# Kernel tuning notes

Hardware: AMD Instinct MI355X
Metric: run time of the kernel (lower is better)

Reference implementation:

```python
import jax, jax.numpy as jnp
import numpy as np

NUM_HEADS = 8
KERNEL = 7  # odd, dilation = 1


def _neighbor_indices(n, k):
    # NATTEN semantics: window start clamped so the kxk window stays inside [0, n)
    r = k // 2
    starts = jnp.clip(jnp.arange(n) - r, 0, n - k)  # [n]
    return starts[:, None] + jnp.arange(k)[None, :]  # [n, k]


def setup_inputs() -> dict:
    key = jax.random.key(0)
    k1, k2, k3, k4 = jax.random.split(key, 4)
    B, H, W, C = 2, 56, 56, 256
    return {
        "x": jax.random.normal(k1, (B, H, W, C), dtype=jnp.float32),
        "w_qk": jax.random.normal(k2, (2 * C, C), dtype=jnp.float32) * 0.02,
        "w_v": jax.random.normal(k3, (C, C), dtype=jnp.float32) * 0.02,
        "w_proj": jax.random.normal(k4, (C, C), dtype=jnp.float32) * 0.02,
        "b_proj": jnp.zeros((C,), dtype=jnp.float32),
    }


def reference(x, w_qk, w_v, w_proj, b_proj):
    B, H, W, C = x.shape
    NH, K = NUM_HEADS, KERNEL
    HD = C // NH
    scale = HD ** -0.5

    # qk / v projections (torch Linear: y = x @ W.T)
    qk = (x @ w_qk.T).reshape(B, H, W, 2, NH, HD)
    q = jnp.moveaxis(qk[:, :, :, 0], 3, 1) * scale  # [B, NH, H, W, HD]
    k = jnp.moveaxis(qk[:, :, :, 1], 3, 1)          # [B, NH, H, W, HD]
    v = jnp.moveaxis((x @ w_v.T).reshape(B, H, W, NH, HD), 3, 1)  # [B, NH, H, W, HD]

    idx_h = _neighbor_indices(H, K)  # [H, K]
    idx_w = _neighbor_indices(W, K)  # [W, K]
    ih = idx_h[:, None, :, None]  # [H, 1, K, 1]
    iw = idx_w[None, :, None, :]  # [1, W, 1, K]

    # Gather per-pixel neighborhoods: [B, NH, H, W, K, K, HD]
    k_nb = k[:, :, ih, iw, :]
    v_nb = v[:, :, ih, iw, :]

    # windowed QK^T -> [B, NH, H, W, K*K]
    attn = jnp.einsum('bnijf,bnijpqf->bnijpq', q, k_nb).reshape(B, NH, H, W, K * K)
    attn = jax.nn.softmax(attn, axis=-1)

    # windowed AV -> [B, NH, H, W, HD]
    out = jnp.einsum('bnijk,bnijkf->bnijf', attn, v_nb.reshape(B, NH, H, W, K * K, HD))

    out = jnp.moveaxis(out, 1, 3).reshape(B, H, W, C)
    out = out @ w_proj.T + b_proj
    return out, attn
```

## Files before the change

kernel.cpp:

```cpp
#include <hip/hip_runtime.h>
#include <math.h>

#define Bb   2
#define Hh   56
#define Ww   56
#define Cc   256
#define NHh  8
#define HDd  32
#define KK   7
#define HWsz (Hh*Ww)
#define Mtot (Bb*Hh*Ww)

typedef __bf16 bf16x8 __attribute__((ext_vector_type(8)));
typedef __bf16 bf16x4 __attribute__((ext_vector_type(4)));
typedef float  f32x4  __attribute__((ext_vector_type(4)));

__global__ __launch_bounds__(256) void prep_bf16(
    const float* __restrict__ x, const float* __restrict__ wqk,
    const float* __restrict__ wv, const float* __restrict__ wp,
    __bf16* __restrict__ xb, __bf16* __restrict__ wallb, __bf16* __restrict__ wpb)
{
    const int t = blockIdx.x * 256 + threadIdx.x;
    const float* src; __bf16* dst; int off;
    if (t < 200704)      { src = x;   dst = xb;             off = t; }
    else if (t < 217088) { src = wqk; dst = wallb;          off = t - 200704; }
    else if (t < 225280) { src = wv;  dst = wallb + 131072; off = t - 217088; }
    else                 { src = wp;  dst = wpb;            off = t - 225280; }
    const int e = off * 8;
    float4 a = *(const float4*)(src + e);
    float4 b = *(const float4*)(src + e + 4);
    bf16x8 o = { (__bf16)a.x, (__bf16)a.y, (__bf16)a.z, (__bf16)a.w,
                 (__bf16)b.x, (__bf16)b.y, (__bf16)b.z, (__bf16)b.w };
    *(bf16x8*)(dst + e) = o;
}

__global__ __launch_bounds__(256) void gemm_qkv_b(
    const __bf16* __restrict__ A, const __bf16* __restrict__ Wall,
    __bf16* __restrict__ Out, float scale)
{
    __shared__ __bf16 As[4096];
    __shared__ __bf16 Bs[4096];

    const int Kdim = 256;
    const int tid = threadIdx.x;
    const int bid = blockIdx.x;
    const int swz = (bid & 7) * 147 + (bid >> 3);
    const int m0  = (swz / 12) * 64;
    const int n0  = (swz % 12) * 64;

    const int mm = tid >> 2;
    const int q  = tid & 3;
    const __bf16* arow = A    + (size_t)(m0 + mm) * Kdim + q * 16;
    const __bf16* brow = Wall + (size_t)(n0 + mm) * Kdim + q * 16;

    const int ks_st  = q >> 1;
    const int sub_st = mm >> 4;
    const int row_st = mm & 15;
    const int c0_st  = (q & 1) * 2;
    const int blk_st = ks_st * 4 + sub_st;
    const int off0 = blk_st * 512 + row_st * 32 + ((c0_st ^ (row_st & 3)) * 8);
    const int off1 = blk_st * 512 + row_st * 32 + (((c0_st + 1) ^ (row_st & 3)) * 8);

    const int w    = tid >> 6;
    const int lane = tid & 63;
    const int fr_row = lane & 15;
    const int fr_c   = lane >> 4;
    const int fr_off = fr_row * 32 + ((fr_c ^ (fr_row & 3)) * 8);

    f32x4 acc[4] = {};

    for (int k0 = 0; k0 < Kdim; k0 += 64) {
        bf16x8 av0 = *(const bf16x8*)(arow + k0);
        bf16x8 av1 = *(const bf16x8*)(arow + k0 + 8);
        bf16x8 bv0 = *(const bf16x8*)(brow + k0);
        bf16x8 bv1 = *(const bf16x8*)(brow + k0 + 8);
        __syncthreads();
        *(bf16x8*)&As[off0] = av0;
        *(bf16x8*)&As[off1] = av1;
        *(bf16x8*)&Bs[off0] = bv0;
        *(bf16x8*)&Bs[off1] = bv1;
        __syncthreads();
        #pragma unroll
        for (int ks = 0; ks < 2; ++ks) {
            bf16x8 af = *(const bf16x8*)&As[(ks * 4 + w) * 512 + fr_off];
            #pragma unroll
            for (int n = 0; n < 4; ++n) {
                bf16x8 bfr = *(const bf16x8*)&Bs[(ks * 4 + n) * 512 + fr_off];
                acc[n] = __builtin_amdgcn_mfma_f32_16x16x32_bf16(af, bfr, acc[n], 0, 0, 0);
            }
        }
    }

    #pragma unroll
    for (int n = 0; n < 4; ++n) {
        const int gcol = n0 + n * 16 + fr_row;
        const float sc_ = (gcol < 256) ? scale : 1.f;
        #pragma unroll
        for (int r = 0; r < 4; ++r) {
            const int grow = m0 + w * 16 + fr_c * 4 + r;
            Out[(size_t)grow * 768 + gcol] = (__bf16)(acc[n][r] * sc_);
        }
    }
}

__global__ __launch_bounds__(256) void gemm_proj_b(
    const __bf16* __restrict__ A, const __bf16* __restrict__ W,
    float* __restrict__ Cout, const float* __restrict__ bias)
{
    __shared__ __bf16 As[4096];
    __shared__ __bf16 Bs[4096];

    const int Kdim = 256, N = 256;
    const int tid = threadIdx.x;
    const int bid = blockIdx.x;
    const int swz = (bid & 7) * 49 + (bid >> 3);
    const int m0  = (swz / 4) * 64;
    const int n0  = (swz % 4) * 64;

    const int mm = tid >> 2;
    const int q  = tid & 3;
    const __bf16* arow = A + (size_t)(m0 + mm) * Kdim + q * 16;
    const __bf16* brow = W + (size_t)(n0 + mm) * Kdim + q * 16;

    const int ks_st  = q >> 1;
    const int sub_st = mm >> 4;
    const int row_st = mm & 15;
    const int c0_st  = (q & 1) * 2;
    const int blk_st = ks_st * 4 + sub_st;
    const int off0 = blk_st * 512 + row_st * 32 + ((c0_st ^ (row_st & 3)) * 8);
    const int off1 = blk_st * 512 + row_st * 32 + (((c0_st + 1) ^ (row_st & 3)) * 8);

    const int w    = tid >> 6;
    const int lane = tid & 63;
    const int fr_row = lane & 15;
    const int fr_c   = lane >> 4;
    const int fr_off = fr_row * 32 + ((fr_c ^ (fr_row & 3)) * 8);

    f32x4 acc[4] = {};

    for (int k0 = 0; k0 < Kdim; k0 += 64) {
        bf16x8 av0 = *(const bf16x8*)(arow + k0);
        bf16x8 av1 = *(const bf16x8*)(arow + k0 + 8);
        bf16x8 bv0 = *(const bf16x8*)(brow + k0);
        bf16x8 bv1 = *(const bf16x8*)(brow + k0 + 8);
        __syncthreads();
        *(bf16x8*)&As[off0] = av0;
        *(bf16x8*)&As[off1] = av1;
        *(bf16x8*)&Bs[off0] = bv0;
        *(bf16x8*)&Bs[off1] = bv1;
        __syncthreads();
        #pragma unroll
        for (int ks = 0; ks < 2; ++ks) {
            bf16x8 af = *(const bf16x8*)&As[(ks * 4 + w) * 512 + fr_off];
            #pragma unroll
            for (int n = 0; n < 4; ++n) {
                bf16x8 bfr = *(const bf16x8*)&Bs[(ks * 4 + n) * 512 + fr_off];
                acc[n] = __builtin_amdgcn_mfma_f32_16x16x32_bf16(af, bfr, acc[n], 0, 0, 0);
            }
        }
    }

    #pragma unroll
    for (int n = 0; n < 4; ++n) {
        const int gcol = n0 + n * 16 + fr_row;
        const float bs_ = bias[gcol];
        #pragma unroll
        for (int r = 0; r < 4; ++r) {
            const int grow = m0 + w * 16 + fr_c * 4 + r;
            Cout[(size_t)grow * N + gcol] = acc[n][r] + bs_;
        }
    }
}

__global__ __launch_bounds__(256, 5) void nattn_84(
    const __bf16* __restrict__ qkv, __bf16* __restrict__ attn_out,
    float* __restrict__ attn_glob)
{
    __shared__ __align__(16) __bf16 Ks[140 * 40];
    __shared__ float Ss[32 * 49];

    const int bid = blockIdx.x;
    const int swz = (bid & 7) * 196 + (bid >> 3);
    const int head = swz & 7;
    int t = swz >> 3;
    const int tj = t % 14; t /= 14;
    const int ti = t % 7;
    const int b  = t / 7;
    const int tid = threadIdx.x;

    int base_h = ti * 8 - 3; if (base_h < 0) base_h = 0; if (base_h > Hh - 14) base_h = Hh - 14;
    int base_w = tj * 4 - 3; if (base_w < 0) base_w = 0; if (base_w > Ww - 10) base_w = Ww - 10;

    const int pixb = b * HWsz;
    const int hoff = head * 32;

    #pragma unroll
    for (int it = 0; it < 3; ++it) {
        const int idx = tid + it * 256;
        if (idx < 560) {
            const int p = idx >> 2, c = idx & 3;
            const int pix = pixb + (base_h + p / 10) * Ww + base_w + p % 10;
            *(bf16x8*)&Ks[p * 40 + c * 8] =
                *(const bf16x8*)&qkv[(size_t)pix * 768 + 256 + hoff + c * 8];
        }
    }

    const int q  = tid >> 3;
    const int r  = tid & 7;
    const int qi = ti * 8 + (q >> 2);
    const int qj = tj * 4 + (q & 3);

    float qreg[32];
    {
        const __bf16* qp = &qkv[(size_t)(pixb + qi * Ww + qj) * 768 + hoff];
        #pragma unroll
        for (int c = 0; c < 4; ++c) {
            bf16x8 qv = *(const bf16x8*)(qp + c * 8);
            #pragma unroll
            for (int j = 0; j < 8; ++j) qreg[c * 8 + j] = (float)qv[j];
        }
    }

    bf16x8 vreg[3];
    #pragma unroll
    for (int it = 0; it < 3; ++it) {
        const int idx = tid + it * 256;
        if (idx < 560) {
            const int p = idx >> 2, c = idx & 3;
            const int pix = pixb + (base_h + p / 10) * Ww + base_w + p % 10;
            vreg[it] = *(const bf16x8*)&qkv[(size_t)pix * 768 + 512 + hoff + c * 8];
        }
    }
    __syncthreads();

    int ih0 = qi - 3; if (ih0 < 0) ih0 = 0; if (ih0 > Hh - 7) ih0 = Hh - 7;
    int iw0 = qj - 3; if (iw0 < 0) iw0 = 0; if (iw0 > Ww - 7) iw0 = Ww - 7;
    const int lh0 = ih0 - base_h, lw0 = iw0 - base_w;

    float sc[7];
    float mx = -1e30f;
    #pragma unroll
    for (int tt = 0; tt < 7; ++tt) {
        const int k = r + 8 * tt;
        if (k < 49) {
            const int krow = (lh0 + k / 7) * 10 + lw0 + k % 7;
            const __bf16* kp = &Ks[krow * 40];
            float acc = 0.f;
            #pragma unroll
            for (int c = 0; c < 4; ++c) {
                bf16x8 kv = *(const bf16x8*)(kp + c * 8);
                #pragma unroll
                for (int j = 0; j < 8; ++j)
                    acc += qreg[c * 8 + j] * (float)kv[j];
            }
            sc[tt] = acc;
            mx = fmaxf(mx, acc);
        }
    }
    mx = fmaxf(mx, __shfl_xor(mx, 1));
    mx = fmaxf(mx, __shfl_xor(mx, 2));
    mx = fmaxf(mx, __shfl_xor(mx, 4));
    float sum = 0.f;
    #pragma unroll
    for (int tt = 0; tt < 7; ++tt) {
        const int k = r + 8 * tt;
        if (k < 49) { sc[tt] = __expf(sc[tt] - mx); sum += sc[tt]; }
    }
    sum += __shfl_xor(sum, 1);
    sum += __shfl_xor(sum, 2);
    sum += __shfl_xor(sum, 4);
    const float inv = 1.f / sum;
    #pragma unroll
    for (int tt = 0; tt < 7; ++tt) {
        const int k = r + 8 * tt;
        if (k < 49) Ss[q * 49 + k] = sc[tt] * inv;
    }
    __syncthreads();

    #pragma unroll
    for (int it = 0; it < 3; ++it) {
        const int idx = tid + it * 256;
        if (idx < 560) {
            const int p = idx >> 2, c = idx & 3;
            *(bf16x8*)&Ks[p * 40 + c * 8] = vreg[it];
        }
    }
    const size_t agbase = (size_t)(b * NHh + head) * HWsz;
    for (int idx = tid; idx < 32 * 49; idx += 256) {
        const int qq = idx / 49, k = idx - qq * 49;
        attn_glob[(agbase + (ti * 8 + (qq >> 2)) * Ww + tj * 4 + (qq & 3)) * 49 + k]
            = Ss[qq * 49 + k];
    }
    __syncthreads();

    const int rc  = r & 3;
    const int par = r >> 2;
    float a[8] = {};
    #pragma unroll
    for (int tt = 0; tt < 25; ++tt) {
        const int k = par + 2 * tt;
        if (k < 49) {
            const float pr = Ss[q * 49 + k];
            const int vrow = (lh0 + k / 7) * 10 + lw0 + k % 7;
            bf16x8 v8 = *(const bf16x8*)&Ks[vrow * 40 + rc * 8];
            #pragma unroll
            for (int j = 0; j < 8; ++j)
                a[j] += pr * (float)v8[j];
        }
    }
    #pragma unroll
    for (int j = 0; j < 8; ++j) a[j] += __shfl_xor(a[j], 4);

    bf16x4 o = { (__bf16)a[par * 4 + 0], (__bf16)a[par * 4 + 1],
                 (__bf16)a[par * 4 + 2], (__bf16)a[par * 4 + 3] };
    *(bf16x4*)(attn_out + (size_t)(pixb + qi * Ww + qj) * 256 + hoff + rc * 8 + par * 4) = o;
}

extern "C" void kernel_launch(void* const* d_in, const int* in_sizes, int n_in,
                              void* d_out, int out_size, void* d_ws, size_t ws_size,
                              hipStream_t stream)
{
    const float* x      = (const float*)d_in[0];
    const float* w_qk   = (const float*)d_in[1];
    const float* w_v    = (const float*)d_in[2];
    const float* w_proj = (const float*)d_in[3];
    const float* b_proj = (const float*)d_in[4];

    float* out       = (float*)d_out;
    float* attn_glob = out + (size_t)Mtot * Cc;

    __bf16* xb      = (__bf16*)d_ws;
    __bf16* wallb   = xb + (size_t)Mtot * 256;
    __bf16* wpb     = wallb + 768 * 256;
    __bf16* qkv_ws  = wpb + 256 * 256;
    __bf16* attn_ws = qkv_ws + (size_t)Mtot * 768;

    const float scale = 0.17677669529663687f;

    prep_bf16<<<912, 256, 0, stream>>>(x, w_qk, w_v, w_proj, xb, wallb, wpb);

    gemm_qkv_b<<<1176, 256, 0, stream>>>(xb, wallb, qkv_ws, scale);

    nattn_84<<<Bb * 7 * 14 * NHh, 256, 0, stream>>>(qkv_ws, attn_ws, attn_glob);

    gemm_proj_b<<<392, 256, 0, stream>>>(attn_ws, wpb, out, b_proj);
}
```

Measured before the change: 106.2 us.

## Enlarge neighborhood-attention tile to 8x8 queries with separate K/V shared buffers

The attention kernel now processes an 8x8 query tile per block instead of 8x4, loading a 14x14 halo of K and V into separate shared buffers at the start. This lowers halo overhead per query and removes the register staging of V, the K-to-V buffer overwrite and one barrier. Each thread now handles 4 lanes per query and computes the full 8-channel AV output itself, so the cross-lane shuffle reduction is gone. In exchange, shared memory per block grows and the occupancy hint drops from 5 to 3 blocks, with half as many blocks in the grid.

Result: no change. 105.6 us (-0.5%).

```diff
diff --git a/kernel.cpp b/kernel.cpp
--- a/kernel.cpp
+++ b/kernel.cpp
@@ -172,43 +172,45 @@
     }
 }
 
-__global__ __launch_bounds__(256, 5) void nattn_84(
+__global__ __launch_bounds__(256, 3) void nattn_88(
     const __bf16* __restrict__ qkv, __bf16* __restrict__ attn_out,
     float* __restrict__ attn_glob)
 {
-    __shared__ __align__(16) __bf16 Ks[140 * 40];
-    __shared__ float Ss[32 * 49];
+    __shared__ __align__(16) __bf16 Ks[196 * 40];
+    __shared__ __align__(16) __bf16 Vs[196 * 40];
+    __shared__ float Ss[64 * 49];
 
     const int bid = blockIdx.x;
-    const int swz = (bid & 7) * 196 + (bid >> 3);
+    const int swz = (bid & 7) * 98 + (bid >> 3);
     const int head = swz & 7;
     int t = swz >> 3;
-    const int tj = t % 14; t /= 14;
+    const int tj = t % 7; t /= 7;
     const int ti = t % 7;
     const int b  = t / 7;
     const int tid = threadIdx.x;
 
     int base_h = ti * 8 - 3; if (base_h < 0) base_h = 0; if (base_h > Hh - 14) base_h = Hh - 14;
-    int base_w = tj * 4 - 3; if (base_w < 0) base_w = 0; if (base_w > Ww - 10) base_w = Ww - 10;
+    int base_w = tj * 8 - 3; if (base_w < 0) base_w = 0; if (base_w > Ww - 14) base_w = Ww - 14;
 
     const int pixb = b * HWsz;
     const int hoff = head * 32;
 
     #pragma unroll
-    for (int it = 0; it < 3; ++it) {
+    for (int it = 0; it < 4; ++it) {
         const int idx = tid + it * 256;
-        if (idx < 560) {
+        if (idx < 784) {
             const int p = idx >> 2, c = idx & 3;
-            const int pix = pixb + (base_h + p / 10) * Ww + base_w + p % 10;
-            *(bf16x8*)&Ks[p * 40 + c * 8] =
-                *(const bf16x8*)&qkv[(size_t)pix * 768 + 256 + hoff + c * 8];
-        }
-    }
-
-    const int q  = tid >> 3;
-    const int r  = tid & 7;
-    const int qi = ti * 8 + (q >> 2);
-    const int qj = tj * 4 + (q & 3);
+            const size_t rb = (size_t)(pixb + (base_h + p / 14) * Ww + base_w + p % 14) * 768
+                              + hoff + c * 8;
+            *(bf16x8*)&Ks[p * 40 + c * 8] = *(const bf16x8*)&qkv[rb + 256];
+            *(bf16x8*)&Vs[p * 40 + c * 8] = *(const bf16x8*)&qkv[rb + 512];
+        }
+    }
+
+    const int q  = tid >> 2;
+    const int r  = tid & 3;
+    const int qi = ti * 8 + (q >> 3);
+    const int qj = tj * 8 + (q & 7);
 
     float qreg[32];
     {
@@ -220,31 +222,19 @@
             for (int j = 0; j < 8; ++j) qreg[c * 8 + j] = (float)qv[j];
         }
     }
-
-    bf16x8 vreg[3];
-    #pragma unroll
-    for (int it = 0; it < 3; ++it) {
-        const int idx = tid + it * 256;
-        if (idx < 560) {
-            const int p = idx >> 2, c = idx & 3;
-            const int pix = pixb + (base_h + p / 10) * Ww + base_w + p % 10;
-            vreg[it] = *(const bf16x8*)&qkv[(size_t)pix * 768 + 512 + hoff + c * 8];
-        }
-    }
     __syncthreads();
 
     int ih0 = qi - 3; if (ih0 < 0) ih0 = 0; if (ih0 > Hh - 7) ih0 = Hh - 7;
     int iw0 = qj - 3; if (iw0 < 0) iw0 = 0; if (iw0 > Ww - 7) iw0 = Ww - 7;
     const int lh0 = ih0 - base_h, lw0 = iw0 - base_w;
 
-    float sc[7];
+    float sc[13];
     float mx = -1e30f;
     #pragma unroll
-    for (int tt = 0; tt < 7; ++tt) {
-        const int k = r + 8 * tt;
+    for (int tt = 0; tt < 13; ++tt) {
+        const int k = r + 4 * tt;
         if (k < 49) {
-            const int krow = (lh0 + k / 7) * 10 + lw0 + k % 7;
-            const __bf16* kp = &Ks[krow * 40];
+            const __bf16* kp = &Ks[((lh0 + k / 7) * 14 + lw0 + k % 7) * 40];
             float acc = 0.f;
             #pragma unroll
             for (int c = 0; c < 4; ++c) {
@@ -259,61 +249,46 @@
     }
     mx = fmaxf(mx, __shfl_xor(mx, 1));
     mx = fmaxf(mx, __shfl_xor(mx, 2));
-    mx = fmaxf(mx, __shfl_xor(mx, 4));
     float sum = 0.f;
     #pragma unroll
-    for (int tt = 0; tt < 7; ++tt) {
-        const int k = r + 8 * tt;
+    for (int tt = 0; tt < 13; ++tt) {
+        const int k = r + 4 * tt;
         if (k < 49) { sc[tt] = __expf(sc[tt] - mx); sum += sc[tt]; }
     }
     sum += __shfl_xor(sum, 1);
     sum += __shfl_xor(sum, 2);
-    sum += __shfl_xor(sum, 4);
     const float inv = 1.f / sum;
     #pragma unroll
-    for (int tt = 0; tt < 7; ++tt) {
-        const int k = r + 8 * tt;
+    for (int tt = 0; tt < 13; ++tt) {
+        const int k = r + 4 * tt;
         if (k < 49) Ss[q * 49 + k] = sc[tt] * inv;
     }
     __syncthreads();
 
-    #pragma unroll
-    for (int it = 0; it < 3; ++it) {
-        const int idx = tid + it * 256;
-        if (idx < 560) {
-            const int p = idx >> 2, c = idx & 3;
-            *(bf16x8*)&Ks[p * 40 + c * 8] = vreg[it];
-        }
-    }
     const size_t agbase = (size_t)(b * NHh + head) * HWsz;
-    for (int idx = tid; idx < 32 * 49; idx += 256) {
+    for (int idx = tid; idx < 64 * 49; idx += 256) {
         const int qq = idx / 49, k = idx - qq * 49;
-        attn_glob[(agbase + (ti * 8 + (qq >> 2)) * Ww + tj * 4 + (qq & 3)) * 49 + k]
+        attn_glob[(agbase + (ti * 8 + (qq >> 3)) * Ww + tj * 8 + (qq & 7)) * 49 + k]
             = Ss[qq * 49 + k];
     }
-    __syncthreads();
-
-    const int rc  = r & 3;
-    const int par = r >> 2;
+
     float a[8] = {};
     #pragma unroll
-    for (int tt = 0; tt < 25; ++tt) {
-        const int k = par + 2 * tt;
-        if (k < 49) {
-            const float pr = Ss[q * 49 + k];
-            const int vrow = (lh0 + k / 7) * 10 + lw0 + k % 7;
-            bf16x8 v8 = *(const bf16x8*)&Ks[vrow * 40 + rc * 8];
+    for (int kh = 0; kh < 7; ++kh) {
+        const __bf16* vrow0 = &Vs[((lh0 + kh) * 14 + lw0) * 40 + r * 8];
+        const float* ps = &Ss[q * 49 + kh * 7];
+        #pragma unroll
+        for (int kw = 0; kw < 7; ++kw) {
+            const float pr = ps[kw];
+            bf16x8 v8 = *(const bf16x8*)(vrow0 + kw * 40);
             #pragma unroll
             for (int j = 0; j < 8; ++j)
                 a[j] += pr * (float)v8[j];
         }
     }
-    #pragma unroll
-    for (int j = 0; j < 8; ++j) a[j] += __shfl_xor(a[j], 4);
-
-    bf16x4 o = { (__bf16)a[par * 4 + 0], (__bf16)a[par * 4 + 1],
-                 (__bf16)a[par * 4 + 2], (__bf16)a[par * 4 + 3] };
-    *(bf16x4*)(attn_out + (size_t)(pixb + qi * Ww + qj) * 256 + hoff + rc * 8 + par * 4) = o;
+    bf16x8 o = { (__bf16)a[0], (__bf16)a[1], (__bf16)a[2], (__bf16)a[3],
+                 (__bf16)a[4], (__bf16)a[5], (__bf16)a[6], (__bf16)a[7] };
+    *(bf16x8*)(attn_out + (size_t)(pixb + qi * Ww + qj) * 256 + hoff + r * 8) = o;
 }
 
 extern "C" void kernel_launch(void* const* d_in, const int* in_sizes, int n_in,
@@ -341,7 +316,7 @@
 
     gemm_qkv_b<<<1176, 256, 0, stream>>>(xb, wallb, qkv_ws, scale);
 
-    nattn_84<<<Bb * 7 * 14 * NHh, 256, 0, stream>>>(qkv_ws, attn_ws, attn_glob);
+    nattn_88<<<784, 256, 0, stream>>>(qkv_ws, attn_ws, attn_glob);
 
     gemm_proj_b<<<392, 256, 0, stream>>>(attn_ws, wpb, out, b_proj);
 }
```
